# Performance work log

Hardware: AMD Instinct MI355X
Metric: run time of the kernel (lower is better)

The kernel has to match this reference:

```python
import jax, jax.numpy as jnp
import numpy as np

B, S, H, P, D = 4, 2048, 2048, 4096, 1024
I = min(1024, P)  # intermediate_dim


def setup_inputs() -> dict:
    key = jax.random.key(0)
    ks = jax.random.split(key, 8)
    sc = lambda n: 1.0 / np.sqrt(n)
    return {
        "x": jax.random.normal(ks[0], (B, S, H), jnp.float32),
        "tensor_pool": jax.random.normal(ks[1], (P, D), jnp.float32),
        "top_k": 2,
        "w1": jax.random.normal(ks[2], (H, I), jnp.float32) * sc(H),
        "b1": jnp.zeros((I,), jnp.float32),
        "w2": jax.random.normal(ks[3], (I, P), jnp.float32) * sc(I),
        "b2": jnp.zeros((P,), jnp.float32),
        "temperature": jnp.float32(0.5),
        "wp": jax.random.normal(ks[4], (H, D), jnp.float32) * sc(H),
        "bp": jnp.zeros((D,), jnp.float32),
        "gamma": jnp.ones((D,), jnp.float32),
        "beta": jnp.zeros((D,), jnp.float32),
        "wm": jax.random.normal(ks[5], (2 * D, D), jnp.float32) * sc(2 * D),
        "bm": jnp.zeros((D,), jnp.float32),
    }


def _layer_norm(h, gamma, beta, eps=1e-5):
    mu = jnp.mean(h, axis=-1, keepdims=True)
    var = jnp.mean(jnp.square(h - mu), axis=-1, keepdims=True)
    return (h - mu) * jax.lax.rsqrt(var + eps) * gamma + beta


def reference(x, tensor_pool, top_k, w1, b1, w2, b2, temperature, wp, bp, gamma, beta, wm, bm):
    pool_size = tensor_pool.shape[0]
    # router MLP
    inter = jax.nn.relu(jnp.einsum('bsh,hi->bsi', x, w1) + b1)
    logits = jnp.einsum('bsi,ip->bsp', inter, w2) + b2
    temp = jnp.clip(temperature, 0.1, 5.0)
    scaled_logits = jnp.clip(logits / temp, -10.0, 10.0)
    # top-k select + softmax over selected
    topk_logits, topk_idx = jax.lax.top_k(scaled_logits, top_k)  # [B,S,K]
    topk_w = jax.nn.softmax(topk_logits, axis=-1)
    # gather pool entries and combine
    experts_out = tensor_pool[topk_idx]                     # [B,S,K,D]
    weighted_map = jnp.einsum('bsk,bskd->bsd', topk_w, experts_out)
    projected_x = _layer_norm(jnp.einsum('bsh,hd->bsd', x, wp) + bp, gamma, beta)
    combined = jnp.concatenate([projected_x, weighted_map], axis=-1)  # [B,S,2D]
    transformation = jnp.einsum('bse,ed->bsd', combined, wm) + bm
    # usage stats via scatter-add
    usage = jnp.zeros((pool_size,), x.dtype).at[topk_idx.reshape(-1)].add(topk_w.reshape(-1))
    usage_fraction = usage / (usage.sum() + 1e-8)
    uniform = 1.0 / pool_size
    scale = min(1.0, x.size / (pool_size * top_k))
    diversity_loss = jnp.mean(jnp.square(usage_fraction - uniform)) * scale * 0.01
    return transformation, diversity_loss
```

## Files before the change

kernel.cpp:

```cpp
#include <hip/hip_runtime.h>
#include <hip/hip_bf16.h>
#include <float.h>
#include <limits.h>

#define NTOK 8192
#define H_   2048
#define P_   4096
#define D_   1024
#define I_   1024

#define MAXC  16
#define DELTA 0.09375f
#define TAU   4.0e-4f
#define FLAGCAP 512

typedef unsigned short ushort_t;
typedef __attribute__((ext_vector_type(8))) short short8;
typedef __attribute__((ext_vector_type(4))) float floatx4;

static __device__ inline ushort_t f2bf(float f) {
    __hip_bfloat16 h = __float2bfloat16(f);
    return *reinterpret_cast<ushort_t*>(&h);
}
static __device__ inline short f2bfs(float f) {
    __hip_bfloat16 h = __float2bfloat16(f);
    return *reinterpret_cast<short*>(&h);
}
static __device__ inline float bf2f(ushort_t s) { return __uint_as_float((unsigned)s << 16); }

static __device__ inline void ins2(float& v0, int& i0, float& v1, int& i1, float v, int i) {
    if (v > v0 || (v == v0 && i < i0)) { v1 = v0; i1 = i0; v0 = v; i0 = i; }
    else if (v > v1 || (v == v1 && i < i1)) { v1 = v; i1 = i; }
}

static __device__ __forceinline__ void gload16(const void* g, void* l) {
    __builtin_amdgcn_global_load_lds(
        (const __attribute__((address_space(1))) unsigned int*)g,
        (__attribute__((address_space(3))) unsigned int*)l,
        16, 0, 0);
}

__global__ __launch_bounds__(256) void split_x(
    const float* __restrict__ in, ushort_t* __restrict__ hi,
    ushort_t* __restrict__ lo, int n4)
{
    int idx = blockIdx.x * 256 + threadIdx.x;
    const int stride = gridDim.x * 256;
    for (; idx < n4; idx += stride) {
        float4 v = ((const float4*)in)[idx];
        ushort4 h, l;
        h.x = f2bf(v.x); l.x = f2bf(v.x - bf2f(h.x));
        h.y = f2bf(v.y); l.y = f2bf(v.y - bf2f(h.y));
        h.z = f2bf(v.z); l.z = f2bf(v.z - bf2f(h.z));
        h.w = f2bf(v.w); l.w = f2bf(v.w - bf2f(h.w));
        ((ushort4*)hi)[idx] = h;
        ((ushort4*)lo)[idx] = l;
    }
}

__global__ __launch_bounds__(256) void prep_weights(
    const float* __restrict__ w2, float* __restrict__ w2tf, ushort_t* __restrict__ w2t,
    const float* __restrict__ wp, ushort_t* __restrict__ wpt,
    const float* __restrict__ wm, ushort_t* __restrict__ wmt,
    const float* __restrict__ w1, ushort_t* __restrict__ w1tHi, ushort_t* __restrict__ w1tLo)
{
    __shared__ float tile[32][33];
    const int tid = threadIdx.x;
    const int tx = tid & 31, ty = tid >> 5;
    int b = blockIdx.x;
    const float* in; int R, Cc, seg, bx, by;
    if (b < 4096)      { seg = 0; in = w2; R = I_; Cc = P_; bx = b & 127; by = b >> 7; }
    else if (b < 6144) { seg = 1; b -= 4096; in = wp; R = H_; Cc = D_; bx = b & 31; by = b >> 5; }
    else if (b < 8192) { seg = 2; b -= 6144; in = wm; R = H_; Cc = D_; bx = b & 31; by = b >> 5; }
    else               { seg = 3; b -= 8192; in = w1; R = H_; Cc = I_; bx = b & 31; by = b >> 5; }
    const int c0 = bx * 32, r0 = by * 32;
#pragma unroll
    for (int j = 0; j < 4; j++)
        tile[ty + j * 8][tx] = in[(size_t)(r0 + ty + j * 8) * Cc + c0 + tx];
    __syncthreads();
#pragma unroll
    for (int j = 0; j < 4; j++) {
        float v = tile[tx][ty + j * 8];
        const size_t o = (size_t)(c0 + ty + j * 8) * R + r0 + tx;
        if (seg == 0)      { w2t[o] = f2bf(v); w2tf[o] = v; }
        else if (seg == 1) { wpt[o] = f2bf(v); }
        else if (seg == 2) { wmt[o] = f2bf(v); }
        else { ushort_t h = f2bf(v); w1tHi[o] = h; w1tLo[o] = f2bf(v - bf2f(h)); }
    }
}

static __device__ __forceinline__ void stage_slot(
    const ushort_t* __restrict__ base, int ld, int r0, int kt, int p,
    ushort_t* __restrict__ lds)
{
    const int row = p >> 2;
    const int chunk = (p ^ (p >> 2)) & 3;
    gload16(base + (size_t)(r0 + row) * ld + kt * 32 + chunk * 8, lds + p * 8);
}

template<int EPI>
__global__ __launch_bounds__(512, 2) void gemm_pipe(
    const ushort_t* __restrict__ A, int lda,
    const ushort_t* __restrict__ Bt, int ldb,
    const float* __restrict__ bias,
    float* __restrict__ Cf, ushort_t* __restrict__ Cb, int ldc, int K)
{
    __shared__ ushort_t sA[3][256 * 32];
    __shared__ ushort_t sB[3][128 * 32];

    const int tid  = threadIdx.x;
    const int wave = tid >> 6, lane = tid & 63;
    const int lr = lane & 15, lq = lane >> 4;
    const int wrow = wave >> 1, wcol = wave & 1;

    const int nwg = gridDim.x * gridDim.y;
    int bid = blockIdx.y * gridDim.x + blockIdx.x;
    bid = (bid & 7) * (nwg >> 3) + (bid >> 3);
    const int bx = bid % gridDim.x, by = bid / gridDim.x;
    const int m0 = by * 256, n0 = bx * 128;
    const int NT = K >> 5;

    floatx4 acc[4][4] = {};

    stage_slot(A,  lda, m0, 0, tid,       &sA[0][0]);
    stage_slot(A,  lda, m0, 0, tid + 512, &sA[0][0]);
    stage_slot(Bt, ldb, n0, 0, tid,       &sB[0][0]);
    stage_slot(A,  lda, m0, 1, tid,       &sA[1][0]);
    stage_slot(A,  lda, m0, 1, tid + 512, &sA[1][0]);
    stage_slot(Bt, ldb, n0, 1, tid,       &sB[1][0]);

    for (int kt = 0; kt < NT; kt++) {
        const int cb = kt % 3;
        const int sbuf = (kt + 2) % 3;
        const bool st = (kt + 2) < NT;
        const ushort_t* __restrict__ sAc = &sA[cb][0];
        const ushort_t* __restrict__ sBc = &sB[cb][0];
        short8 bF[4];

#pragma unroll
        for (int p = 0; p < 2; p++) {
            if (p == 0) {
                if (kt + 1 < NT) asm volatile("s_waitcnt vmcnt(3)" ::: "memory");
                else             asm volatile("s_waitcnt vmcnt(0)" ::: "memory");
            }
            __builtin_amdgcn_s_barrier();
            short8 aF[2];
#pragma unroll
            for (int t = 0; t < 2; t++) {
                const int row = wrow * 64 + (2 * p + t) * 16 + lr;
                const int ph = row * 4 + (lq ^ (row & 3));
                aF[t] = *(const short8*)&sAc[ph * 8];
            }
            if (p == 0) {
#pragma unroll
                for (int f = 0; f < 4; f++) {
                    const int row = wcol * 64 + f * 16 + lr;
                    const int ph = row * 4 + (lq ^ (row & 3));
                    bF[f] = *(const short8*)&sBc[ph * 8];
                }
            }
            if (st) {
                if (p == 0) {
                    stage_slot(A,  lda, m0, kt + 2, tid, &sA[sbuf][0]);
                    stage_slot(Bt, ldb, n0, kt + 2, tid, &sB[sbuf][0]);
                } else {
                    stage_slot(A,  lda, m0, kt + 2, tid + 512, &sA[sbuf][0]);
                }
            }
            __builtin_amdgcn_s_setprio(1);
#pragma unroll
            for (int t = 0; t < 2; t++)
#pragma unroll
                for (int j = 0; j < 4; j++)
                    acc[2 * p + t][j] = __builtin_amdgcn_mfma_f32_16x16x32_bf16(
                        aF[t], bF[j], acc[2 * p + t][j], 0, 0, 0);
            __builtin_amdgcn_s_setprio(0);
        }
    }

#pragma unroll
    for (int j = 0; j < 4; j++) {
        const int col = n0 + wcol * 64 + j * 16 + lr;
        const float bv = bias[col];
#pragma unroll
        for (int i = 0; i < 4; i++) {
            const int rowb = m0 + wrow * 64 + i * 16 + lq * 4;
#pragma unroll
            for (int r = 0; r < 4; r++) {
                float v = acc[i][j][r] + bv;
                if (EPI == 1) Cb[(size_t)(rowb + r) * ldc + col] = f2bf(v);
                else          Cf[(size_t)(rowb + r) * ldc + col] = v;
            }
        }
    }
}

__global__ __launch_bounds__(512, 2) void gemm_pipe_split(
    const ushort_t* __restrict__ AH, const ushort_t* __restrict__ AL, int lda,
    const ushort_t* __restrict__ BtH, const ushort_t* __restrict__ BtL, int ldb,
    const float* __restrict__ bias,
    float* __restrict__ Cf, ushort_t* __restrict__ Cb, int ldc, int K)
{
    __shared__ ushort_t sAh[3][256 * 32];
    __shared__ ushort_t sAl[3][256 * 32];
    __shared__ ushort_t sBh[3][128 * 32];
    __shared__ ushort_t sBl[3][128 * 32];

    const int tid  = threadIdx.x;
    const int wave = tid >> 6, lane = tid & 63;
    const int lr = lane & 15, lq = lane >> 4;
    const int wrow = wave >> 1, wcol = wave & 1;

    const int nwg = gridDim.x * gridDim.y;
    int bid = blockIdx.y * gridDim.x + blockIdx.x;
    bid = (bid & 7) * (nwg >> 3) + (bid >> 3);
    const int bx = bid % gridDim.x, by = bid / gridDim.x;
    const int m0 = by * 256, n0 = bx * 128;
    const int NT = K >> 5;

    floatx4 acc[4][4] = {};

#pragma unroll
    for (int t = 0; t < 2; t++) {
        stage_slot(AH,  lda, m0, t, tid,       &sAh[t][0]);
        stage_slot(AH,  lda, m0, t, tid + 512, &sAh[t][0]);
        stage_slot(AL,  lda, m0, t, tid,       &sAl[t][0]);
        stage_slot(AL,  lda, m0, t, tid + 512, &sAl[t][0]);
        stage_slot(BtH, ldb, n0, t, tid,       &sBh[t][0]);
        stage_slot(BtL, ldb, n0, t, tid,       &sBl[t][0]);
    }

    for (int kt = 0; kt < NT; kt++) {
        const int cb = kt % 3;
        const int sbuf = (kt + 2) % 3;
        const bool st = (kt + 2) < NT;
        const ushort_t* __restrict__ sAhc = &sAh[cb][0];
        const ushort_t* __restrict__ sAlc = &sAl[cb][0];
        const ushort_t* __restrict__ sBhc = &sBh[cb][0];
        const ushort_t* __restrict__ sBlc = &sBl[cb][0];
        short8 bH[4], bL[4];

#pragma unroll
        for (int p = 0; p < 2; p++) {
            if (p == 0) {
                if (kt + 1 < NT) asm volatile("s_waitcnt vmcnt(6)" ::: "memory");
                else             asm volatile("s_waitcnt vmcnt(0)" ::: "memory");
            }
            __builtin_amdgcn_s_barrier();
            short8 aH[2], aL[2];
#pragma unroll
            for (int t = 0; t < 2; t++) {
                const int row = wrow * 64 + (2 * p + t) * 16 + lr;
                const int ph = (row * 4 + (lq ^ (row & 3))) * 8;
                aH[t] = *(const short8*)&sAhc[ph];
                aL[t] = *(const short8*)&sAlc[ph];
            }
            if (p == 0) {
#pragma unroll
                for (int f = 0; f < 4; f++) {
                    const int row = wcol * 64 + f * 16 + lr;
                    const int ph = (row * 4 + (lq ^ (row & 3))) * 8;
                    bH[f] = *(const short8*)&sBhc[ph];
                    bL[f] = *(const short8*)&sBlc[ph];
                }
            }
            if (st) {
                if (p == 0) {
                    stage_slot(AH,  lda, m0, kt + 2, tid, &sAh[sbuf][0]);
                    stage_slot(AL,  lda, m0, kt + 2, tid, &sAl[sbuf][0]);
                    stage_slot(BtH, ldb, n0, kt + 2, tid, &sBh[sbuf][0]);
                } else {
                    stage_slot(AH,  lda, m0, kt + 2, tid + 512, &sAh[sbuf][0]);
                    stage_slot(AL,  lda, m0, kt + 2, tid + 512, &sAl[sbuf][0]);
                    stage_slot(BtL, ldb, n0, kt + 2, tid, &sBl[sbuf][0]);
                }
            }
            __builtin_amdgcn_s_setprio(1);
#pragma unroll
            for (int t = 0; t < 2; t++)
#pragma unroll
                for (int j = 0; j < 4; j++) {
                    acc[2 * p + t][j] = __builtin_amdgcn_mfma_f32_16x16x32_bf16(
                        aH[t], bH[j], acc[2 * p + t][j], 0, 0, 0);
                    acc[2 * p + t][j] = __builtin_amdgcn_mfma_f32_16x16x32_bf16(
                        aH[t], bL[j], acc[2 * p + t][j], 0, 0, 0);
                    acc[2 * p + t][j] = __builtin_amdgcn_mfma_f32_16x16x32_bf16(
                        aL[t], bH[j], acc[2 * p + t][j], 0, 0, 0);
                }
            __builtin_amdgcn_s_setprio(0);
        }
    }

#pragma unroll
    for (int j = 0; j < 4; j++) {
        const int col = n0 + wcol * 64 + j * 16 + lr;
        const float bv = bias[col];
#pragma unroll
        for (int i = 0; i < 4; i++) {
            const int rowb = m0 + wrow * 64 + i * 16 + lq * 4;
#pragma unroll
            for (int r = 0; r < 4; r++) {
                float v = fmaxf(acc[i][j][r] + bv, 0.f);
                Cf[(size_t)(rowb + r) * ldc + col] = v;
                Cb[(size_t)(rowb + r) * ldc + col] = f2bf(v);
            }
        }
    }
}

template<int ASRC, int EPI>
__global__ __launch_bounds__(256) void gemm_lds(
    const void* __restrict__ Av, int lda,
    const ushort_t* __restrict__ Bt, int ldb,
    const float* __restrict__ bias,
    float* __restrict__ Cf, ushort_t* __restrict__ Cb, int ldc, int K)
{
    __shared__ ushort_t sA[128 * 32];
    __shared__ ushort_t sB[128 * 32];

    const int tid  = threadIdx.x;
    const int wave = tid >> 6, lane = tid & 63;
    const int lr = lane & 15, lq = lane >> 4;

    const int nwg = gridDim.x * gridDim.y;
    int bid = blockIdx.y * gridDim.x + blockIdx.x;
    bid = (bid & 7) * (nwg >> 3) + (bid >> 3);
    const int bx = bid % gridDim.x, by = bid / gridDim.x;
    const int m0 = by * 128, n0 = bx * 128;
    const int m0w = m0 + (wave >> 1) * 64, n0w = n0 + (wave & 1) * 64;

    const int n1 = tid, n2 = tid + 256;

    floatx4 acc[4][4] = {};

    for (int k0 = 0; k0 < K; k0 += 32) {
        __syncthreads();
        gload16(Bt + (size_t)(n0 + (n1 >> 2)) * ldb + k0 + (n1 & 3) * 8, &sB[n1 * 8]);
        gload16(Bt + (size_t)(n0 + (n2 >> 2)) * ldb + k0 + (n2 & 3) * 8, &sB[n2 * 8]);
        if (ASRC == 1) {
            const ushort_t* Ab = (const ushort_t*)Av;
            gload16(Ab + (size_t)(m0 + (n1 >> 2)) * lda + k0 + (n1 & 3) * 8, &sA[n1 * 8]);
            gload16(Ab + (size_t)(m0 + (n2 >> 2)) * lda + k0 + (n2 & 3) * 8, &sA[n2 * 8]);
        } else {
#pragma unroll
            for (int ss = 0; ss < 2; ss++) {
                const int s = tid + ss * 256;
                const float* ap = (const float*)Av + (size_t)(m0 + (s >> 2)) * lda + k0 + (s & 3) * 8;
                float4 v0 = *(const float4*)ap;
                float4 v1 = *(const float4*)(ap + 4);
                short8 h;
                h[0] = f2bfs(v0.x); h[1] = f2bfs(v0.y); h[2] = f2bfs(v0.z); h[3] = f2bfs(v0.w);
                h[4] = f2bfs(v1.x); h[5] = f2bfs(v1.y); h[6] = f2bfs(v1.z); h[7] = f2bfs(v1.w);
                *(short8*)&sA[s * 8] = h;
            }
        }
        __syncthreads();

        short8 aF[4], bF[4];
#pragma unroll
        for (int f = 0; f < 4; f++) {
            const int ra = ((wave >> 1) * 64 + f * 16 + lr) * 32 + lq * 8;
            aF[f] = *(const short8*)&sA[ra];
            const int rb = ((wave & 1) * 64 + f * 16 + lr) * 32 + lq * 8;
            bF[f] = *(const short8*)&sB[rb];
        }
#pragma unroll
        for (int i = 0; i < 4; i++)
#pragma unroll
            for (int j = 0; j < 4; j++)
                acc[i][j] = __builtin_amdgcn_mfma_f32_16x16x32_bf16(aF[i], bF[j], acc[i][j], 0, 0, 0);
    }

#pragma unroll
    for (int j = 0; j < 4; j++) {
        const int col = n0w + j * 16 + lr;
        const float bv = bias[col];
#pragma unroll
        for (int i = 0; i < 4; i++) {
            const int rowb = m0w + i * 16 + lq * 4;
#pragma unroll
            for (int r = 0; r < 4; r++) {
                float v = acc[i][j][r] + bv;
                if (EPI == 1) Cb[(size_t)(rowb + r) * ldc + col] = f2bf(v);
                else          Cf[(size_t)(rowb + r) * ldc + col] = v;
            }
        }
    }
}

__global__ __launch_bounds__(256) void cand_scan(
    const ushort_t* __restrict__ logitsb,
    int* __restrict__ cidx, int* __restrict__ ccnt)
{
    __shared__ float sv0[4], sv1[4];
    __shared__ int   scnt;
    const int tok = blockIdx.x;
    const int tid = threadIdx.x;
    const ushort_t* row = logitsb + (size_t)tok * P_;

    float my[16];
    {
        const uint4* rp = (const uint4*)(row + tid * 16);
        uint4 u0 = rp[0], u1 = rp[1];
        unsigned w[8] = {u0.x, u0.y, u0.z, u0.w, u1.x, u1.y, u1.z, u1.w};
#pragma unroll
        for (int j = 0; j < 8; j++) {
            my[2 * j]     = __uint_as_float(w[j] << 16);
            my[2 * j + 1] = __uint_as_float(w[j] & 0xFFFF0000u);
        }
    }
    float v0 = -FLT_MAX, v1 = -FLT_MAX;
#pragma unroll
    for (int j = 0; j < 16; j++) {
        float v = my[j];
        if (v > v0) { v1 = v0; v0 = v; } else if (v > v1) v1 = v;
    }
#pragma unroll
    for (int off = 1; off < 64; off <<= 1) {
        float u0 = __shfl_xor(v0, off), u1 = __shfl_xor(v1, off);
        float n0 = fmaxf(v0, u0);
        float n1 = fmaxf(fminf(v0, u0), fmaxf(v1, u1));
        v0 = n0; v1 = n1;
    }
    const int wv = tid >> 6;
    if ((tid & 63) == 0) { sv0[wv] = v0; sv1[wv] = v1; }
    if (tid == 0) scnt = 0;
    __syncthreads();
    float g0 = -FLT_MAX, g1 = -FLT_MAX;
#pragma unroll
    for (int w = 0; w < 4; w++) {
        float u0 = sv0[w], u1 = sv1[w];
        float n0 = fmaxf(g0, u0);
        float n1 = fmaxf(fminf(g0, u0), fmaxf(g1, u1));
        g0 = n0; g1 = n1;
    }
    const float thresh = g1 - DELTA;
#pragma unroll
    for (int j = 0; j < 16; j++) {
        if (my[j] >= thresh) {
            int pos = atomicAdd(&scnt, 1);
            if (pos < MAXC) cidx[tok * MAXC + pos] = tid * 16 + j;
        }
    }
    __syncthreads();
    if (tid == 0) ccnt[tok] = min(scnt, MAXC);
}

__global__ __launch_bounds__(256) void recheck(
    const float* __restrict__ interf, const float* __restrict__ w2tf,
    const float* __restrict__ b2, const int* __restrict__ cidx,
    const int* __restrict__ ccnt, const float* __restrict__ temp_p,
    int2* __restrict__ tki, float2* __restrict__ tkw,
    int* __restrict__ flagcnt, int* __restrict__ flaglist)
{
    __shared__ double ex[MAXC];
    __shared__ int    sidx[MAXC];
    const int tok  = blockIdx.x;
    const int tid  = threadIdx.x;
    const int wave = tid >> 6, lane = tid & 63;
    int cnt = min(max(ccnt[tok], 0), MAXC);

    const float* ir = interf + (size_t)tok * I_;
    for (int c = wave; c < cnt; c += 4) {
        int p = min(max(cidx[tok * MAXC + c], 0), P_ - 1);
        const float* wr = w2tf + (size_t)p * I_;
        double s = 0.0;
        for (int k = lane; k < I_; k += 64)
            s += (double)ir[k] * (double)wr[k];
#pragma unroll
        for (int off = 32; off; off >>= 1) s += __shfl_down(s, off);
        if (lane == 0) { ex[c] = s + (double)b2[p]; sidx[c] = p; }
    }
    __syncthreads();
    if (tid == 0) {
        float v0 = -FLT_MAX, v1 = -FLT_MAX; int i0 = INT_MAX, i1 = INT_MAX;
        for (int c = 0; c < cnt; c++) ins2(v0, i0, v1, i1, (float)ex[c], sidx[c]);
        if (i0 == INT_MAX) { i0 = 0; v0 = 0.f; }
        if (i1 == INT_MAX) { i1 = i0; v1 = v0; }
        if (cnt >= 3) {
            float v2 = -FLT_MAX;
            for (int c = 0; c < cnt; c++) {
                if (sidx[c] == i0 || sidx[c] == i1) continue;
                float v = (float)ex[c];
                if (v > v2) v2 = v;
            }
            if (v1 - v2 < TAU) {
                int pos = atomicAdd(flagcnt, 1);
                if (pos < FLAGCAP) flaglist[pos] = tok;
            }
        }
        float tc = fminf(fmaxf(temp_p[0], 0.1f), 5.0f);
        float s0 = fminf(fmaxf(v0 / tc, -10.f), 10.f);
        float s1 = fminf(fmaxf(v1 / tc, -10.f), 10.f);
        float m  = fmaxf(s0, s1);
        float e0 = expf(s0 - m), e1 = expf(s1 - m);
        float inv = 1.0f / (e0 + e1);
        tki[tok] = make_int2(i0, i1);
        tkw[tok] = make_float2(e0 * inv, e1 * inv);
    }
}

__global__ __launch_bounds__(256) void fallback_gemv(
    const float* __restrict__ x, const float* __restrict__ w1,
    const int* __restrict__ flagcnt, const int* __restrict__ flaglist,
    double* __restrict__ part)
{
    __shared__ float sx[128];
    const int tid = threadIdx.x;
    const int nf = min(flagcnt[0], FLAGCAP);
    const int nitems = nf * 16;

    for (int idx = blockIdx.x; idx < nitems; idx += gridDim.x) {
        const int fi = idx >> 4, slice = idx & 15;
        const int tok = flaglist[fi];
        const int h0 = slice * 128;
        __syncthreads();
        if (tid < 128) sx[tid] = x[(size_t)tok * H_ + h0 + tid];
        __syncthreads();

        const int col = tid * 4;
        double a0 = 0.0, a1 = 0.0, a2 = 0.0, a3 = 0.0;
        for (int h = 0; h < 128; h += 8) {
            float4 wv[8];
#pragma unroll
            for (int u = 0; u < 8; u++)
                wv[u] = *(const float4*)(w1 + (size_t)(h0 + h + u) * I_ + col);
#pragma unroll
            for (int u = 0; u < 8; u++) {
                const double xv = (double)sx[h + u];
                a0 += xv * (double)wv[u].x;
                a1 += xv * (double)wv[u].y;
                a2 += xv * (double)wv[u].z;
                a3 += xv * (double)wv[u].w;
            }
        }
        double* pp = part + ((size_t)fi * 16 + slice) * I_ + col;
        pp[0] = a0; pp[1] = a1; pp[2] = a2; pp[3] = a3;
    }
}

__global__ __launch_bounds__(256) void fallback_reduce(
    const double* __restrict__ part, const float* __restrict__ b1,
    const float* __restrict__ w2tf, const float* __restrict__ b2,
    const int* __restrict__ cidx, const int* __restrict__ ccnt,
    const int* __restrict__ flagcnt, const int* __restrict__ flaglist,
    const float* __restrict__ temp_p,
    int2* __restrict__ tki, float2* __restrict__ tkw)
{
    __shared__ double sInter[I_];
    __shared__ double ex[MAXC];
    __shared__ int    sidx[MAXC];
    const int tid  = threadIdx.x;
    const int wave = tid >> 6, lane = tid & 63;
    const int nf = min(flagcnt[0], FLAGCAP);

    for (int fi = blockIdx.x; fi < nf; fi += gridDim.x) {
        const int tok = flaglist[fi];
        __syncthreads();
#pragma unroll
        for (int q = 0; q < 4; q++) {
            const int i = q * 256 + tid;
            double v = (double)b1[i];
            const double* pp = part + (size_t)fi * 16 * I_ + i;
#pragma unroll
            for (int s = 0; s < 16; s++) v += pp[(size_t)s * I_];
            sInter[i] = v > 0.0 ? v : 0.0;
        }
        __syncthreads();

        const int cnt = min(max(ccnt[tok], 0), MAXC);
        for (int c = wave; c < cnt; c += 4) {
            int p = min(max(cidx[tok * MAXC + c], 0), P_ - 1);
            const float* wr = w2tf + (size_t)p * I_;
            double s = 0.0;
            for (int k = lane; k < I_; k += 64)
                s += sInter[k] * (double)wr[k];
#pragma unroll
            for (int off = 32; off; off >>= 1) s += __shfl_down(s, off);
            if (lane == 0) { ex[c] = s + (double)b2[p]; sidx[c] = p; }
        }
        __syncthreads();
        if (tid == 0) {
            float v0 = -FLT_MAX, v1 = -FLT_MAX; int i0 = INT_MAX, i1 = INT_MAX;
            for (int c = 0; c < cnt; c++) ins2(v0, i0, v1, i1, (float)ex[c], sidx[c]);
            if (i0 == INT_MAX) { i0 = 0; v0 = 0.f; }
            if (i1 == INT_MAX) { i1 = i0; v1 = v0; }
            float tc = fminf(fmaxf(temp_p[0], 0.1f), 5.0f);
            float s0 = fminf(fmaxf(v0 / tc, -10.f), 10.f);
            float s1 = fminf(fmaxf(v1 / tc, -10.f), 10.f);
            float m  = fmaxf(s0, s1);
            float e0 = expf(s0 - m), e1 = expf(s1 - m);
            float inv = 1.0f / (e0 + e1);
            tki[tok] = make_int2(i0, i1);
            tkw[tok] = make_float2(e0 * inv, e1 * inv);
        }
    }
}

static __device__ inline float blockReduceSum256(float v, float* red) {
#pragma unroll
    for (int off = 32; off; off >>= 1) v += __shfl_down(v, off);
    const int wv = threadIdx.x >> 6;
    if ((threadIdx.x & 63) == 0) red[wv] = v;
    __syncthreads();
    float tot = red[0] + red[1] + red[2] + red[3];
    __syncthreads();
    return tot;
}

__global__ __launch_bounds__(256) void build_combined(
    const float* __restrict__ proj, ushort_t* __restrict__ comb,
    const float* __restrict__ pool,
    const float* __restrict__ gamma, const float* __restrict__ beta,
    const int2* __restrict__ tki, const float2* __restrict__ tkw,
    float* __restrict__ usage)
{
    __shared__ float red[4];
    const int tok = blockIdx.x;
    const int tid = threadIdx.x;
    const int c = tid * 4;

    float4 v = *(const float4*)&proj[(size_t)tok * D_ + c];
    float s = v.x + v.y + v.z + v.w;
    float tot = blockReduceSum256(s, red);
    float mu = tot * (1.0f / D_);
    float d0 = v.x - mu, d1 = v.y - mu, d2 = v.z - mu, d3 = v.w - mu;
    float sq = d0 * d0 + d1 * d1 + d2 * d2 + d3 * d3;
    float var = blockReduceSum256(sq, red) * (1.0f / D_);
    float rs = 1.0f / sqrtf(var + 1e-5f);

    float4 g  = *(const float4*)&gamma[c];
    float4 be = *(const float4*)&beta[c];
    ushort4 o;
    o.x = f2bf(d0 * rs * g.x + be.x);
    o.y = f2bf(d1 * rs * g.y + be.y);
    o.z = f2bf(d2 * rs * g.z + be.z);
    o.w = f2bf(d3 * rs * g.w + be.w);
    *(ushort4*)&comb[(size_t)tok * (2 * D_) + c] = o;

    int2   ii = tki[tok];
    int ia = min(max(ii.x, 0), P_ - 1);
    int ib = min(max(ii.y, 0), P_ - 1);
    float2 ww = tkw[tok];
    float4 p0 = *(const float4*)&pool[(size_t)ia * D_ + c];
    float4 p1 = *(const float4*)&pool[(size_t)ib * D_ + c];
    ushort4 wm;
    wm.x = f2bf(ww.x * p0.x + ww.y * p1.x);
    wm.y = f2bf(ww.x * p0.y + ww.y * p1.y);
    wm.z = f2bf(ww.x * p0.z + ww.y * p1.z);
    wm.w = f2bf(ww.x * p0.w + ww.y * p1.w);
    *(ushort4*)&comb[(size_t)tok * (2 * D_) + D_ + c] = wm;

    if (tid == 0) {
        atomicAdd(&usage[ia], ww.x);
        atomicAdd(&usage[ib], ww.y);
    }
}

__global__ __launch_bounds__(256) void diversity_kernel(
    const float* __restrict__ usage, float* __restrict__ out)
{
    __shared__ float red[4];
    const int tid = threadIdx.x;
    float s = 0.f;
    for (int j = tid; j < P_; j += 256) s += usage[j];
    float tot = blockReduceSum256(s, red) + 1e-8f;
    float q = 0.f;
    const float uni = 1.0f / P_;
    for (int j = tid; j < P_; j += 256) {
        float f = usage[j] / tot - uni;
        q += f * f;
    }
    float ssq = blockReduceSum256(q, red);
    if (tid == 0) out[(size_t)NTOK * D_] = ssq * (1.0f / P_) * 0.01f;
}

extern "C" void kernel_launch(void* const* d_in, const int* in_sizes, int n_in,
                              void* d_out, int out_size, void* d_ws, size_t ws_size,
                              hipStream_t stream) {
    const float* x     = (const float*)d_in[0];
    const float* pool  = (const float*)d_in[1];
    const float* w1    = (const float*)d_in[3];
    const float* b1    = (const float*)d_in[4];
    const float* w2    = (const float*)d_in[5];
    const float* b2    = (const float*)d_in[6];
    const float* temp  = (const float*)d_in[7];
    const float* wp    = (const float*)d_in[8];
    const float* bp    = (const float*)d_in[9];
    const float* gamma = (const float*)d_in[10];
    const float* beta  = (const float*)d_in[11];
    const float* wm    = (const float*)d_in[12];
    const float* bm    = (const float*)d_in[13];
    float* out = (float*)d_out;

    float* ws = (float*)d_ws;
    const size_t MF = (size_t)1024 * 1024;
    float*    interf  = ws;
    ushort_t* interb  = (ushort_t*)(ws + 8 * MF);
    ushort_t* xHi     = (ushort_t*)(ws + 12 * MF);
    ushort_t* xLo     = (ushort_t*)(ws + 20 * MF);
    ushort_t* logitsb = (ushort_t*)(ws + 12 * MF);
    double*   part    = (double*)(ws + 12 * MF);
    float*    projb   = ws + 12 * MF;
    ushort_t* comb    = (ushort_t*)(ws + 20 * MF);
    float*    w2tf    = ws + 28 * MF;
    ushort_t* w2t     = (ushort_t*)(ws + 32 * MF);
    ushort_t* wpt     = (ushort_t*)(ws + 34 * MF);
    ushort_t* wmt     = (ushort_t*)(ws + 35 * MF);
    ushort_t* w1tHi   = (ushort_t*)(ws + 36 * MF);
    ushort_t* w1tLo   = (ushort_t*)(ws + 37 * MF);
    int*      cidx    = (int*)(ws + 38 * MF);
    int*      ccnt    = cidx + NTOK * MAXC;
    int2*     tki     = (int2*)(ccnt + NTOK);
    float2*   tkw     = (float2*)(tki + NTOK);
    float*    usage   = (float*)(tkw + NTOK);
    int*      flagcnt = (int*)(usage + P_);
    int*      flaglist= flagcnt + 1;

    hipMemsetAsync(usage, 0, (P_ + 1) * sizeof(float), stream);

    dim3 blk(256);
    prep_weights<<<10240, blk, 0, stream>>>(w2, w2tf, w2t, wp, wpt, wm, wmt,
                                            w1, w1tHi, w1tLo);

    split_x<<<2048, blk, 0, stream>>>(x, xHi, xLo, NTOK * H_ / 4);

    gemm_pipe_split<<<dim3(I_ / 128, NTOK / 256), dim3(512), 0, stream>>>(
        xHi, xLo, H_, w1tHi, w1tLo, H_, b1, interf, interb, I_, H_);

    gemm_pipe<1><<<dim3(P_ / 128, NTOK / 256), dim3(512), 0, stream>>>(
        interb, I_, w2t, I_, b2, nullptr, logitsb, P_, I_);

    cand_scan<<<NTOK, blk, 0, stream>>>(logitsb, cidx, ccnt);
    recheck<<<NTOK, blk, 0, stream>>>(interf, w2tf, b2, cidx, ccnt, temp, tki, tkw,
                                      flagcnt, flaglist);

    fallback_gemv<<<1024, blk, 0, stream>>>(x, w1, flagcnt, flaglist, part);
    fallback_reduce<<<128, blk, 0, stream>>>(part, b1, w2tf, b2, cidx, ccnt,
                                             flagcnt, flaglist, temp, tki, tkw);

    gemm_lds<0, 0><<<dim3(D_ / 128, NTOK / 128), blk, 0, stream>>>(
        x, H_, wpt, H_, bp, projb, nullptr, D_, H_);

    build_combined<<<NTOK, blk, 0, stream>>>(projb, comb, pool, gamma, beta, tki, tkw, usage);

    gemm_pipe<0><<<dim3(D_ / 128, NTOK / 256), dim3(512), 0, stream>>>(
        comb, 2 * D_, wmt, 2 * D_, bm, out, nullptr, D_, 2 * D_);

    diversity_kernel<<<1, blk, 0, stream>>>(usage, out);
}
```

Baseline: 591.6 us.

## Fuse fp32-to-bf16 hi/lo split of x into GEMM loaders; pipeline projection GEMM

Removes the separate split_x pass. The router's first GEMM now loads fp32 x through registers and converts it to bf16 hi/lo parts while writing LDS, prefetching one k-tile ahead. The projection GEMM moves from the simple single-buffered gemm_lds to a triple-buffered 256x128 pipelined kernel with the same register-side fp32 conversion. This saves writing and re-reading the 64MB hi/lo x buffers, but adds VGPR pressure and conversion ALU work inside the GEMM main loop.

```diff
diff --git a/kernel.cpp b/kernel.cpp
--- a/kernel.cpp
+++ b/kernel.cpp
@@ -38,24 +38,6 @@
         (const __attribute__((address_space(1))) unsigned int*)g,
         (__attribute__((address_space(3))) unsigned int*)l,
         16, 0, 0);
-}
-
-__global__ __launch_bounds__(256) void split_x(
-    const float* __restrict__ in, ushort_t* __restrict__ hi,
-    ushort_t* __restrict__ lo, int n4)
-{
-    int idx = blockIdx.x * 256 + threadIdx.x;
-    const int stride = gridDim.x * 256;
-    for (; idx < n4; idx += stride) {
-        float4 v = ((const float4*)in)[idx];
-        ushort4 h, l;
-        h.x = f2bf(v.x); l.x = f2bf(v.x - bf2f(h.x));
-        h.y = f2bf(v.y); l.y = f2bf(v.y - bf2f(h.y));
-        h.z = f2bf(v.z); l.z = f2bf(v.z - bf2f(h.z));
-        h.w = f2bf(v.w); l.w = f2bf(v.w - bf2f(h.w));
-        ((ushort4*)hi)[idx] = h;
-        ((ushort4*)lo)[idx] = l;
-    }
 }
 
 __global__ __launch_bounds__(256) void prep_weights(
@@ -98,6 +80,30 @@
     gload16(base + (size_t)(r0 + row) * ld + kt * 32 + chunk * 8, lds + p * 8);
 }
 
+static __device__ __forceinline__ void cvt_write_hl(
+    float4 v0, float4 v1, ushort_t* dh, ushort_t* dl)
+{
+    float fb[8] = {v0.x, v0.y, v0.z, v0.w, v1.x, v1.y, v1.z, v1.w};
+    short8 h, l;
+#pragma unroll
+    for (int e = 0; e < 8; e++) {
+        short hh = f2bfs(fb[e]);
+        h[e] = hh;
+        l[e] = f2bfs(fb[e] - bf2f((ushort_t)hh));
+    }
+    *(short8*)dh = h;
+    *(short8*)dl = l;
+}
+static __device__ __forceinline__ void cvt_write_h(
+    float4 v0, float4 v1, ushort_t* dh)
+{
+    float fb[8] = {v0.x, v0.y, v0.z, v0.w, v1.x, v1.y, v1.z, v1.w};
+    short8 h;
+#pragma unroll
+    for (int e = 0; e < 8; e++) h[e] = f2bfs(fb[e]);
+    *(short8*)dh = h;
+}
+
 template<int EPI>
 __global__ __launch_bounds__(512, 2) void gemm_pipe(
     const ushort_t* __restrict__ A, int lda,
@@ -195,8 +201,8 @@
     }
 }
 
-__global__ __launch_bounds__(512, 2) void gemm_pipe_split(
-    const ushort_t* __restrict__ AH, const ushort_t* __restrict__ AL, int lda,
+__global__ __launch_bounds__(512, 2) void gemm_pipe_split_rs(
+    const float* __restrict__ A, int lda,
     const ushort_t* __restrict__ BtH, const ushort_t* __restrict__ BtL, int ldb,
     const float* __restrict__ bias,
     float* __restrict__ Cf, ushort_t* __restrict__ Cb, int ldc, int K)
@@ -218,22 +224,33 @@
     const int m0 = by * 256, n0 = bx * 128;
     const int NT = K >> 5;
 
+    const int p1 = tid, p2 = tid + 512;
+    const float* a1p = A + (size_t)(m0 + (p1 >> 2)) * lda + ((p1 ^ (p1 >> 2)) & 3) * 8;
+    const float* a2p = A + (size_t)(m0 + (p2 >> 2)) * lda + ((p2 ^ (p2 >> 2)) & 3) * 8;
+
     floatx4 acc[4][4] = {};
-
-#pragma unroll
-    for (int t = 0; t < 2; t++) {
-        stage_slot(AH,  lda, m0, t, tid,       &sAh[t][0]);
-        stage_slot(AH,  lda, m0, t, tid + 512, &sAh[t][0]);
-        stage_slot(AL,  lda, m0, t, tid,       &sAl[t][0]);
-        stage_slot(AL,  lda, m0, t, tid + 512, &sAl[t][0]);
-        stage_slot(BtH, ldb, n0, t, tid,       &sBh[t][0]);
-        stage_slot(BtL, ldb, n0, t, tid,       &sBl[t][0]);
-    }
+    float4 xa0, xa1, xb0, xb1;
+
+    stage_slot(BtH, ldb, n0, 0, tid, &sBh[0][0]);
+    stage_slot(BtL, ldb, n0, 0, tid, &sBl[0][0]);
+    stage_slot(BtH, ldb, n0, 1, tid, &sBh[1][0]);
+    stage_slot(BtL, ldb, n0, 1, tid, &sBl[1][0]);
+    {
+        float4 t0 = *(const float4*)(a1p);
+        float4 t1 = *(const float4*)(a1p + 4);
+        float4 t2 = *(const float4*)(a2p);
+        float4 t3 = *(const float4*)(a2p + 4);
+        cvt_write_hl(t0, t1, &sAh[0][p1 * 8], &sAl[0][p1 * 8]);
+        cvt_write_hl(t2, t3, &sAh[0][p2 * 8], &sAl[0][p2 * 8]);
+    }
+    xa0 = *(const float4*)(a1p + 32);
+    xa1 = *(const float4*)(a1p + 36);
+    xb0 = *(const float4*)(a2p + 32);
+    xb1 = *(const float4*)(a2p + 36);
 
     for (int kt = 0; kt < NT; kt++) {
-        const int cb = kt % 3;
-        const int sbuf = (kt + 2) % 3;
-        const bool st = (kt + 2) < NT;
+        const int cb = kt % 3, sbuf = (kt + 2) % 3, wbuf = (kt + 1) % 3;
+        const bool st1 = (kt + 1) < NT, st2 = (kt + 2) < NT;
         const ushort_t* __restrict__ sAhc = &sAh[cb][0];
         const ushort_t* __restrict__ sAlc = &sAl[cb][0];
         const ushort_t* __restrict__ sBhc = &sBh[cb][0];
@@ -243,8 +260,9 @@
 #pragma unroll
         for (int p = 0; p < 2; p++) {
             if (p == 0) {
-                if (kt + 1 < NT) asm volatile("s_waitcnt vmcnt(6)" ::: "memory");
-                else             asm volatile("s_waitcnt vmcnt(0)" ::: "memory");
+                if (st1) asm volatile("s_waitcnt vmcnt(6)" ::: "memory");
+                else     asm volatile("s_waitcnt vmcnt(0)" ::: "memory");
+                asm volatile("s_waitcnt lgkmcnt(0)" ::: "memory");
             }
             __builtin_amdgcn_s_barrier();
             short8 aH[2], aL[2];
@@ -263,16 +281,20 @@
                     bH[f] = *(const short8*)&sBhc[ph];
                     bL[f] = *(const short8*)&sBlc[ph];
                 }
-            }
-            if (st) {
-                if (p == 0) {
-                    stage_slot(AH,  lda, m0, kt + 2, tid, &sAh[sbuf][0]);
-                    stage_slot(AL,  lda, m0, kt + 2, tid, &sAl[sbuf][0]);
+                if (st2) {
                     stage_slot(BtH, ldb, n0, kt + 2, tid, &sBh[sbuf][0]);
-                } else {
-                    stage_slot(AH,  lda, m0, kt + 2, tid + 512, &sAh[sbuf][0]);
-                    stage_slot(AL,  lda, m0, kt + 2, tid + 512, &sAl[sbuf][0]);
                     stage_slot(BtL, ldb, n0, kt + 2, tid, &sBl[sbuf][0]);
+                }
+            } else {
+                if (st1) {
+                    cvt_write_hl(xa0, xa1, &sAh[wbuf][p1 * 8], &sAl[wbuf][p1 * 8]);
+                    cvt_write_hl(xb0, xb1, &sAh[wbuf][p2 * 8], &sAl[wbuf][p2 * 8]);
+                }
+                if (st2) {
+                    xa0 = *(const float4*)(a1p + (kt + 2) * 32);
+                    xa1 = *(const float4*)(a1p + (kt + 2) * 32 + 4);
+                    xb0 = *(const float4*)(a2p + (kt + 2) * 32);
+                    xb1 = *(const float4*)(a2p + (kt + 2) * 32 + 4);
                 }
             }
             __builtin_amdgcn_s_setprio(1);
@@ -308,82 +330,112 @@
     }
 }
 
-template<int ASRC, int EPI>
-__global__ __launch_bounds__(256) void gemm_lds(
-    const void* __restrict__ Av, int lda,
+__global__ __launch_bounds__(512, 2) void gemm_pipe_f32a(
+    const float* __restrict__ A, int lda,
     const ushort_t* __restrict__ Bt, int ldb,
     const float* __restrict__ bias,
-    float* __restrict__ Cf, ushort_t* __restrict__ Cb, int ldc, int K)
-{
-    __shared__ ushort_t sA[128 * 32];
-    __shared__ ushort_t sB[128 * 32];
+    float* __restrict__ Cf, int ldc, int K)
+{
+    __shared__ ushort_t sA[3][256 * 32];
+    __shared__ ushort_t sB[3][128 * 32];
 
     const int tid  = threadIdx.x;
     const int wave = tid >> 6, lane = tid & 63;
     const int lr = lane & 15, lq = lane >> 4;
+    const int wrow = wave >> 1, wcol = wave & 1;
 
     const int nwg = gridDim.x * gridDim.y;
     int bid = blockIdx.y * gridDim.x + blockIdx.x;
     bid = (bid & 7) * (nwg >> 3) + (bid >> 3);
     const int bx = bid % gridDim.x, by = bid / gridDim.x;
-    const int m0 = by * 128, n0 = bx * 128;
-    const int m0w = m0 + (wave >> 1) * 64, n0w = n0 + (wave & 1) * 64;
-
-    const int n1 = tid, n2 = tid + 256;
+    const int m0 = by * 256, n0 = bx * 128;
+    const int NT = K >> 5;
+
+    const int p1 = tid, p2 = tid + 512;
+    const float* a1p = A + (size_t)(m0 + (p1 >> 2)) * lda + ((p1 ^ (p1 >> 2)) & 3) * 8;
+    const float* a2p = A + (size_t)(m0 + (p2 >> 2)) * lda + ((p2 ^ (p2 >> 2)) & 3) * 8;
 
     floatx4 acc[4][4] = {};
-
-    for (int k0 = 0; k0 < K; k0 += 32) {
-        __syncthreads();
-        gload16(Bt + (size_t)(n0 + (n1 >> 2)) * ldb + k0 + (n1 & 3) * 8, &sB[n1 * 8]);
-        gload16(Bt + (size_t)(n0 + (n2 >> 2)) * ldb + k0 + (n2 & 3) * 8, &sB[n2 * 8]);
-        if (ASRC == 1) {
-            const ushort_t* Ab = (const ushort_t*)Av;
-            gload16(Ab + (size_t)(m0 + (n1 >> 2)) * lda + k0 + (n1 & 3) * 8, &sA[n1 * 8]);
-            gload16(Ab + (size_t)(m0 + (n2 >> 2)) * lda + k0 + (n2 & 3) * 8, &sA[n2 * 8]);
-        } else {
-#pragma unroll
-            for (int ss = 0; ss < 2; ss++) {
-                const int s = tid + ss * 256;
-                const float* ap = (const float*)Av + (size_t)(m0 + (s >> 2)) * lda + k0 + (s & 3) * 8;
-                float4 v0 = *(const float4*)ap;
-                float4 v1 = *(const float4*)(ap + 4);
-                short8 h;
-                h[0] = f2bfs(v0.x); h[1] = f2bfs(v0.y); h[2] = f2bfs(v0.z); h[3] = f2bfs(v0.w);
-                h[4] = f2bfs(v1.x); h[5] = f2bfs(v1.y); h[6] = f2bfs(v1.z); h[7] = f2bfs(v1.w);
-                *(short8*)&sA[s * 8] = h;
-            }
-        }
-        __syncthreads();
-
-        short8 aF[4], bF[4];
-#pragma unroll
-        for (int f = 0; f < 4; f++) {
-            const int ra = ((wave >> 1) * 64 + f * 16 + lr) * 32 + lq * 8;
-            aF[f] = *(const short8*)&sA[ra];
-            const int rb = ((wave & 1) * 64 + f * 16 + lr) * 32 + lq * 8;
-            bF[f] = *(const short8*)&sB[rb];
-        }
-#pragma unroll
-        for (int i = 0; i < 4; i++)
-#pragma unroll
-            for (int j = 0; j < 4; j++)
-                acc[i][j] = __builtin_amdgcn_mfma_f32_16x16x32_bf16(aF[i], bF[j], acc[i][j], 0, 0, 0);
+    float4 xa0, xa1, xb0, xb1;
+
+    stage_slot(Bt, ldb, n0, 0, tid, &sB[0][0]);
+    stage_slot(Bt, ldb, n0, 1, tid, &sB[1][0]);
+    {
+        float4 t0 = *(const float4*)(a1p);
+        float4 t1 = *(const float4*)(a1p + 4);
+        float4 t2 = *(const float4*)(a2p);
+        float4 t3 = *(const float4*)(a2p + 4);
+        cvt_write_h(t0, t1, &sA[0][p1 * 8]);
+        cvt_write_h(t2, t3, &sA[0][p2 * 8]);
+    }
+    xa0 = *(const float4*)(a1p + 32);
+    xa1 = *(const float4*)(a1p + 36);
+    xb0 = *(const float4*)(a2p + 32);
+    xb1 = *(const float4*)(a2p + 36);
+
+    for (int kt = 0; kt < NT; kt++) {
+        const int cb = kt % 3, sbuf = (kt + 2) % 3, wbuf = (kt + 1) % 3;
+        const bool st1 = (kt + 1) < NT, st2 = (kt + 2) < NT;
+        const ushort_t* __restrict__ sAc = &sA[cb][0];
+        const ushort_t* __restrict__ sBc = &sB[cb][0];
+        short8 bF[4];
+
+#pragma unroll
+        for (int p = 0; p < 2; p++) {
+            if (p == 0) {
+                if (st1) asm volatile("s_waitcnt vmcnt(5)" ::: "memory");
+                else     asm volatile("s_waitcnt vmcnt(0)" ::: "memory");
+                asm volatile("s_waitcnt lgkmcnt(0)" ::: "memory");
+            }
+            __builtin_amdgcn_s_barrier();
+            short8 aF[2];
+#pragma unroll
+            for (int t = 0; t < 2; t++) {
+                const int row = wrow * 64 + (2 * p + t) * 16 + lr;
+                const int ph = row * 4 + (lq ^ (row & 3));
+                aF[t] = *(const short8*)&sAc[ph * 8];
+            }
+            if (p == 0) {
+#pragma unroll
+                for (int f = 0; f < 4; f++) {
+                    const int row = wcol * 64 + f * 16 + lr;
+                    const int ph = row * 4 + (lq ^ (row & 3));
+                    bF[f] = *(const short8*)&sBc[ph * 8];
+                }
+                if (st2) stage_slot(Bt, ldb, n0, kt + 2, tid, &sB[sbuf][0]);
+            } else {
+                if (st1) {
+                    cvt_write_h(xa0, xa1, &sA[wbuf][p1 * 8]);
+                    cvt_write_h(xb0, xb1, &sA[wbuf][p2 * 8]);
+                }
+                if (st2) {
+                    xa0 = *(const float4*)(a1p + (kt + 2) * 32);
+                    xa1 = *(const float4*)(a1p + (kt + 2) * 32 + 4);
+                    xb0 = *(const float4*)(a2p + (kt + 2) * 32);
+                    xb1 = *(const float4*)(a2p + (kt + 2) * 32 + 4);
+                }
+            }
+            __builtin_amdgcn_s_setprio(1);
+#pragma unroll
+            for (int t = 0; t < 2; t++)
+#pragma unroll
+                for (int j = 0; j < 4; j++)
+                    acc[2 * p + t][j] = __builtin_amdgcn_mfma_f32_16x16x32_bf16(
+                        aF[t], bF[j], acc[2 * p + t][j], 0, 0, 0);
+            __builtin_amdgcn_s_setprio(0);
+        }
     }
 
 #pragma unroll
     for (int j = 0; j < 4; j++) {
-        const int col = n0w + j * 16 + lr;
+        const int col = n0 + wcol * 64 + j * 16 + lr;
         const float bv = bias[col];
 #pragma unroll
         for (int i = 0; i < 4; i++) {
-            const int rowb = m0w + i * 16 + lq * 4;
-#pragma unroll
-            for (int r = 0; r < 4; r++) {
-                float v = acc[i][j][r] + bv;
-                if (EPI == 1) Cb[(size_t)(rowb + r) * ldc + col] = f2bf(v);
-                else          Cf[(size_t)(rowb + r) * ldc + col] = v;
-            }
+            const int rowb = m0 + wrow * 64 + i * 16 + lq * 4;
+#pragma unroll
+            for (int r = 0; r < 4; r++)
+                Cf[(size_t)(rowb + r) * ldc + col] = acc[i][j][r] + bv;
         }
     }
 }
@@ -697,8 +749,6 @@
     const size_t MF = (size_t)1024 * 1024;
     float*    interf  = ws;
     ushort_t* interb  = (ushort_t*)(ws + 8 * MF);
-    ushort_t* xHi     = (ushort_t*)(ws + 12 * MF);
-    ushort_t* xLo     = (ushort_t*)(ws + 20 * MF);
     ushort_t* logitsb = (ushort_t*)(ws + 12 * MF);
     double*   part    = (double*)(ws + 12 * MF);
     float*    projb   = ws + 12 * MF;
@@ -723,10 +773,8 @@
     prep_weights<<<10240, blk, 0, stream>>>(w2, w2tf, w2t, wp, wpt, wm, wmt,
                                             w1, w1tHi, w1tLo);
 
-    split_x<<<2048, blk, 0, stream>>>(x, xHi, xLo, NTOK * H_ / 4);
-
-    gemm_pipe_split<<<dim3(I_ / 128, NTOK / 256), dim3(512), 0, stream>>>(
-        xHi, xLo, H_, w1tHi, w1tLo, H_, b1, interf, interb, I_, H_);
+    gemm_pipe_split_rs<<<dim3(I_ / 128, NTOK / 256), dim3(512), 0, stream>>>(
+        x, H_, w1tHi, w1tLo, H_, b1, interf, interb, I_, H_);
 
     gemm_pipe<1><<<dim3(P_ / 128, NTOK / 256), dim3(512), 0, stream>>>(
         interb, I_, w2t, I_, b2, nullptr, logitsb, P_, I_);
@@ -739,8 +787,8 @@
     fallback_reduce<<<128, blk, 0, stream>>>(part, b1, w2tf, b2, cidx, ccnt,
                                              flagcnt, flaglist, temp, tki, tkw);
 
-    gemm_lds<0, 0><<<dim3(D_ / 128, NTOK / 128), blk, 0, stream>>>(
-        x, H_, wpt, H_, bp, projb, nullptr, D_, H_);
+    gemm_pipe_f32a<<<dim3(D_ / 128, NTOK / 256), dim3(512), 0, stream>>>(
+        x, H_, wpt, H_, bp, projb, D_, H_);
 
     build_combined<<<NTOK, blk, 0, stream>>>(projb, comb, pool, gamma, beta, tki, tkw, usage);
 
```

After: 555.4 us. 6.1% less time.
